# Kernel tuning notes

Hardware: AMD Instinct MI355X
Metric: run time of the kernel (lower is better)

Reference implementation:

```python
import jax, jax.numpy as jnp
import numpy as np
import math

B, T, E = 2, 2048, 1024
H = 16
D = E // H  # head_dim = 64

def setup_inputs() -> dict:
    key = jax.random.key(0)
    k1, k2, k3, k4, k5 = jax.random.split(key, 5)
    s = 0.02
    return {
        "x": jax.random.normal(k1, (B, T, E), dtype=jnp.float32),
        "W_attn": jax.random.normal(k2, (E, 3 * E), dtype=jnp.float32) * s,
        "b_attn": jax.random.normal(k3, (3 * E,), dtype=jnp.float32) * s,
        "W_proj": jax.random.normal(k4, (E, E), dtype=jnp.float32) * s,
        "b_proj": jax.random.normal(k5, (E,), dtype=jnp.float32) * s,
    }

def reference(x, W_attn, b_attn, W_proj, b_proj):
    Bx, Tx, Ex = x.shape
    qkv = x @ W_attn + b_attn                      # [B,T,3E]
    q, k, v = jnp.split(qkv, 3, axis=2)
    # [B,T,E] -> [B,H,T,D]
    def heads(t):
        return t.reshape(Bx, Tx, H, D).transpose(0, 2, 1, 3)
    q, k, v = heads(q), heads(k), heads(v)
    scores = jnp.einsum('bhqd,bhkd->bhqk', q, k) / math.sqrt(D)
    causal = jnp.tril(jnp.ones((Tx, Tx), dtype=bool))
    scores = jnp.where(causal, scores, -jnp.inf)
    attn = jax.nn.softmax(scores, axis=-1)
    out = jnp.einsum('bhqk,bhkd->bhqd', attn, v)   # [B,H,T,D]
    out = out.transpose(0, 2, 1, 3).reshape(Bx, Tx, Ex)
    return out @ W_proj + b_proj
```

## Files before the change

### kernel.cpp

```cpp
#include <hip/hip_runtime.h>


typedef unsigned short u16;
typedef __bf16 bf8 __attribute__((ext_vector_type(8)));
typedef float f32x4 __attribute__((ext_vector_type(4)));

struct __align__(8) u16x4s { u16 v[4]; };

__device__ __forceinline__ u16 f2b(float f) {
    union { float f; unsigned u; } x{f};
    unsigned r = x.u + 0x7fffu + ((x.u >> 16) & 1u);
    return (u16)(r >> 16);
}

__device__ __forceinline__ f32x4 mfma16(bf8 a, bf8 b, f32x4 c) {
    return __builtin_amdgcn_mfma_f32_16x16x32_bf16(a, b, c, 0, 0, 0);
}

__device__ __forceinline__ float fexp2(float x) {
    return __builtin_amdgcn_exp2f(x);
}

__device__ __forceinline__ void gload_lds16(const u16* g, u16* l) {
    __builtin_amdgcn_global_load_lds(
        (__attribute__((address_space(1))) void*)(g),
        (__attribute__((address_space(3))) void*)(l), 16, 0, 0);
}

__global__ __launch_bounds__(256) void k_prep(const float* __restrict__ x,
                                              const float* __restrict__ Wa,
                                              const float* __restrict__ Wp,
                                              u16* __restrict__ Xb,
                                              u16* __restrict__ WtA,
                                              u16* __restrict__ WtP) {
    __shared__ float tile[64][65];
    int id = blockIdx.x, t = threadIdx.x;
    if (id < 4096) {
        int i = id * 256 + t;
        float4 v = ((const float4*)x)[i];
        ushort4 o;
        o.x = f2b(v.x); o.y = f2b(v.y); o.z = f2b(v.z); o.w = f2b(v.w);
        ((ushort4*)Xb)[i] = o;
        return;
    }
    const float* in; u16* out; int N, j;
    if (id < 4864) { j = id - 4096; in = Wa; out = WtA; N = 3072; }
    else           { j = id - 4864; in = Wp; out = WtP; N = 1024; }
    int k0 = (j & 15) * 64, n0 = (j >> 4) * 64;
    int c = t & 63, r0 = t >> 6;
#pragma unroll
    for (int i = 0; i < 16; ++i) {
        int r = r0 + i * 4;
        tile[r][c] = in[(size_t)(k0 + r) * N + n0 + c];
    }
    __syncthreads();
#pragma unroll
    for (int i = 0; i < 16; ++i) {
        int r = r0 + i * 4;
        out[(size_t)(n0 + r) * 1024 + k0 + c] = f2b(tile[c][r]);
    }
}

#define GEMM_STAGE(GA0, GA1, GB0, GB1, K, B)                                   \
    do {                                                                       \
        gload_lds16(GA0 + (K), As[B] + tid * 8);                               \
        gload_lds16(GA1 + (K), As[B] + (256 + tid) * 8);                       \
        gload_lds16(GB0 + (K), Bs[B] + tid * 8);                               \
        gload_lds16(GB1 + (K), Bs[B] + (256 + tid) * 8);                       \
    } while (0)

#define GEMM_CORE(Aptr, Bptr)                                                  \
    int tid = threadIdx.x;                                                     \
    int w = tid >> 6, lane = tid & 63, l16 = lane & 15, quad = lane >> 4;      \
    int m0 = blockIdx.x * 128, n0 = blockIdx.y * 128;                          \
    int wr = (w >> 1) * 64, wc = (w & 1) * 64;                                 \
    __shared__ u16 As[2][128 * 32];                                            \
    __shared__ u16 Bs[2][128 * 32];                                            \
    f32x4 acc[4][4];                                                           \
    _Pragma("unroll") for (int mi = 0; mi < 4; ++mi)                           \
        _Pragma("unroll") for (int ni = 0; ni < 4; ++ni)                       \
            _Pragma("unroll") for (int r = 0; r < 4; ++r) acc[mi][ni][r] = 0.f;\
    int srow0 = tid >> 2, srow1 = 64 + srow0;                                  \
    int slc = ((tid & 3) ^ ((tid >> 3) & 3)) * 8;      \
    const u16* gA0 = Aptr + (size_t)(m0 + srow0) * 1024 + slc;                 \
    const u16* gA1 = Aptr + (size_t)(m0 + srow1) * 1024 + slc;                 \
    const u16* gB0 = Bptr + (size_t)(n0 + srow0) * 1024 + slc;                 \
    const u16* gB1 = Bptr + (size_t)(n0 + srow1) * 1024 + slc;                 \
    int cq = (quad ^ ((l16 >> 1) & 3)) * 8;               \
    GEMM_STAGE(gA0, gA1, gB0, gB1, 0, 0);                                      \
    for (int it = 0; it < 32; ++it) {                                          \
        int pb = it & 1;                                                       \
        __syncthreads();                           \
        bf8 af[4], bf[4];                                                      \
        _Pragma("unroll") for (int mi = 0; mi < 4; ++mi)                       \
            af[mi] = *(const bf8*)(As[pb] + (wr + mi * 16 + l16) * 32 + cq);   \
        _Pragma("unroll") for (int ni = 0; ni < 4; ++ni)                       \
            bf[ni] = *(const bf8*)(Bs[pb] + (wc + ni * 16 + l16) * 32 + cq);   \
        if (it < 31) GEMM_STAGE(gA0, gA1, gB0, gB1, (it + 1) * 32, pb ^ 1);    \
        _Pragma("unroll") for (int mi = 0; mi < 4; ++mi)                       \
            _Pragma("unroll") for (int ni = 0; ni < 4; ++ni)                   \
                acc[mi][ni] = mfma16(af[mi], bf[ni], acc[mi][ni]);             \
    }

__global__ __launch_bounds__(256, 3) void k_qkv(const u16* __restrict__ Xb,
                                                const u16* __restrict__ WtA,
                                                const float* __restrict__ ba,
                                                u16* __restrict__ Qb,
                                                u16* __restrict__ Kb,
                                                u16* __restrict__ Vtb) {
    GEMM_CORE(Xb, WtA)
    int sel = n0 >> 10;
    u16* dst = sel == 0 ? Qb : (sel == 1 ? Kb : Vtb);
    const float qs = 0.18033688011112042f;
#pragma unroll
    for (int ni = 0; ni < 4; ++ni) {
        int n = n0 + wc + ni * 16 + l16;
        float bias = ba[n];
        int h = (n & 1023) >> 6;
        int d = n & 63;
#pragma unroll
        for (int mi = 0; mi < 4; ++mi)
#pragma unroll
            for (int r = 0; r < 4; ++r) {
                int m = m0 + wr + mi * 16 + quad * 4 + r;
                int bb = m >> 11, tt = m & 2047;
                float v = acc[mi][ni][r] + bias;
                size_t hb = (size_t)(bb * 16 + h);
                if (sel == 2)
                    dst[hb * 131072 + (size_t)(tt >> 6) * 4096 + d * 64 + (tt & 63)] = f2b(v);
                else
                    dst[(hb * 2048 + tt) * 64 + d] =
                        f2b(sel == 0 ? v * qs : v);
            }
    }
}

__global__ __launch_bounds__(256, 3) void k_proj(const u16* __restrict__ AO,
                                                 const u16* __restrict__ WtP,
                                                 const float* __restrict__ bp,
                                                 float* __restrict__ out) {
    GEMM_CORE(AO, WtP)
#pragma unroll
    for (int ni = 0; ni < 4; ++ni) {
        int n = n0 + wc + ni * 16 + l16;
        float bias = bp[n];
#pragma unroll
        for (int mi = 0; mi < 4; ++mi)
#pragma unroll
            for (int r = 0; r < 4; ++r) {
                int m = m0 + wr + mi * 16 + quad * 4 + r;
                out[(size_t)m * 1024 + n] = acc[mi][ni][r] + bias;
            }
    }
}


#define STAGE(KT, B) do {                                                     \
    int ci0_ = tid, ci1_ = 256 + tid;                                         \
    const u16* kt_ = Kh + (size_t)(KT) * 4096;                                \
    gload_lds16(kt_ + (ci0_ >> 3) * 64 +                                      \
                (((ci0_ & 7) ^ ((ci0_ >> 5) & 7)) * 8), Ks[B] + ci0_ * 8);    \
    gload_lds16(kt_ + (ci1_ >> 3) * 64 +                                      \
                (((ci1_ & 7) ^ ((ci1_ >> 5) & 7)) * 8), Ks[B] + ci1_ * 8);    \
    const u16* vt_ = Vh + (size_t)(KT) * 4096;                                \
    gload_lds16(vt_ + (ci0_ >> 3) * 64 +                                      \
                (((ci0_ & 7) ^ ((ci0_ >> 3) & 7)) * 8), Vs[B] + ci0_ * 8);    \
    gload_lds16(vt_ + (ci1_ >> 3) * 64 +                                      \
                (((ci1_ & 7) ^ ((ci1_ >> 3) & 7)) * 8), Vs[B] + ci1_ * 8);    \
} while (0)

#define QK_SOFT(KT, KF, QF0, QF1, LI, QROW, KTM, PBUF) do {                   \
    int kb_ = (KT) * 64;                                                      \
    bool diag_ = ((KT) == (KTM));                                             \
    f32x4 s_acc[4];                                                           \
    _Pragma("unroll") for (int s = 0; s < 4; ++s)                             \
        _Pragma("unroll") for (int r = 0; r < 4; ++r) s_acc[s][r] = 0.f;      \
    _Pragma("unroll") for (int sub = 0; sub < 4; ++sub) {                     \
        s_acc[sub] = mfma16(QF0, KF[sub][0], s_acc[sub]);                     \
        s_acc[sub] = mfma16(QF1, KF[sub][1], s_acc[sub]);                     \
    }                                                                         \
    _Pragma("unroll") for (int r = 0; r < 4; ++r) {                           \
        float p[4];                                                           \
        if (diag_) {                                                          \
            int qg_ = (QROW) + quad * 4 + r;                                  \
            _Pragma("unroll") for (int sub = 0; sub < 4; ++sub) {             \
                int key_ = kb_ + 4 * l16 + sub;                               \
                p[sub] = fexp2(key_ <= qg_ ? s_acc[sub][r] : -1e30f);         \
            }                                                                 \
        } else {                                                              \
            _Pragma("unroll") for (int sub = 0; sub < 4; ++sub)               \
                p[sub] = fexp2(s_acc[sub][r]);                                \
        }                                                                     \
        LI[r] += (p[0] + p[1]) + (p[2] + p[3]);                               \
        u16x4s pk_;                                                           \
        _Pragma("unroll") for (int sub = 0; sub < 4; ++sub)                   \
            pk_.v[sub] = f2b(p[sub]);                                         \
        *(u16x4s*)&PBUF[quad * 4 + r][l16 * 4] = pk_;       \
    }                                                                         \
} while (0)

#define PV_ACC(VF, PBUF, OACC) do {                                           \
    bf8 pf0 = *(const bf8*)&PBUF[l16][quad * 8];                              \
    bf8 pf1 = *(const bf8*)&PBUF[l16][32 + quad * 8];                         \
    _Pragma("unroll") for (int dt = 0; dt < 4; ++dt) {                        \
        OACC[dt] = mfma16(pf0, VF[dt][0], OACC[dt]);                          \
        OACC[dt] = mfma16(pf1, VF[dt][1], OACC[dt]);                          \
    }                                                                         \
} while (0)

__global__ __launch_bounds__(256, 2) void k_attn(const u16* __restrict__ Qb,
                                                 const u16* __restrict__ Kb,
                                                 const u16* __restrict__ Vtb,
                                                 u16* __restrict__ AO) {
    int id = blockIdx.x;
    int bh = (id & 7) * 4 + ((id >> 3) & 3);
    int t  = 15 - (id >> 5);
    int tid = threadIdx.x;
    int w = tid >> 6, lane = tid & 63, l16 = lane & 15, quad = lane >> 4;

    const u16* Qh = Qb  + (size_t)bh * 2048 * 64;
    const u16* Kh = Kb  + (size_t)bh * 2048 * 64;
    const u16* Vh = Vtb + (size_t)bh * 131072;

    int qrA = t * 64 + w * 16;
    int qrB = qrA + 1024;
    int ktmaxA = t, ktmaxB = t + 16;

    __shared__ u16 Ks[2][64 * 64];
    __shared__ u16 Vs[2][64 * 64];
    __shared__ u16 P[4][2][16][72];

    bf8 qfA0 = *(const bf8*)(Qh + (size_t)(qrA + l16) * 64 + quad * 8);
    bf8 qfA1 = *(const bf8*)(Qh + (size_t)(qrA + l16) * 64 + 32 + quad * 8);
    bf8 qfB0 = *(const bf8*)(Qh + (size_t)(qrB + l16) * 64 + quad * 8);
    bf8 qfB1 = *(const bf8*)(Qh + (size_t)(qrB + l16) * 64 + 32 + quad * 8);

    float l_iA[4] = {0.f, 0.f, 0.f, 0.f};
    float l_iB[4] = {0.f, 0.f, 0.f, 0.f};
    f32x4 o_accA[4], o_accB[4];
#pragma unroll
    for (int dt = 0; dt < 4; ++dt)
#pragma unroll
        for (int r = 0; r < 4; ++r) { o_accA[dt][r] = 0.f; o_accB[dt][r] = 0.f; }

    int xsw = (l16 & 7) * 8;

    STAGE(0, 0);
    for (int kt = 0; kt <= ktmaxB; ++kt) {
        int pb = kt & 1;
        __syncthreads();

        bf8 kf[4][2], vf[4][2];
        const u16* kb_ = Ks[pb];
        const u16* vb_ = Vs[pb];
#pragma unroll
        for (int sub = 0; sub < 4; ++sub)
#pragma unroll
            for (int ks = 0; ks < 2; ++ks)
                kf[sub][ks] = *(const bf8*)(kb_ + (4 * l16 + sub) * 64 +
                                            (((ks * 32 + quad * 8)) ^ xsw));
#pragma unroll
        for (int dt = 0; dt < 4; ++dt)
#pragma unroll
            for (int ks = 0; ks < 2; ++ks)
                vf[dt][ks] = *(const bf8*)(vb_ + (dt * 16 + l16) * 64 +
                                           (((ks * 32 + quad * 8)) ^ xsw));

        if (kt < ktmaxB) STAGE(kt + 1, pb ^ 1);

        bool aAct = (kt <= ktmaxA);
        if (aAct) QK_SOFT(kt, kf, qfA0, qfA1, l_iA, qrA, ktmaxA, P[w][0]);
        QK_SOFT(kt, kf, qfB0, qfB1, l_iB, qrB, ktmaxB, P[w][1]);
        asm volatile("s_waitcnt lgkmcnt(0)" ::: "memory");
        if (aAct) PV_ACC(vf, P[w][0], o_accA);
        PV_ACC(vf, P[w][1], o_accB);
    }

    float linvA[4], linvB[4];
#pragma unroll
    for (int r = 0; r < 4; ++r) {
        float la = l_iA[r], lb = l_iB[r];
        la += __shfl_xor(la, 1, 64); lb += __shfl_xor(lb, 1, 64);
        la += __shfl_xor(la, 2, 64); lb += __shfl_xor(lb, 2, 64);
        la += __shfl_xor(la, 4, 64); lb += __shfl_xor(lb, 4, 64);
        la += __shfl_xor(la, 8, 64); lb += __shfl_xor(lb, 8, 64);
        linvA[r] = __builtin_amdgcn_rcpf(la);
        linvB[r] = __builtin_amdgcn_rcpf(lb);
    }

    int b = bh >> 4, h = bh & 15;
#pragma unroll
    for (int dt = 0; dt < 4; ++dt)
#pragma unroll
        for (int r = 0; r < 4; ++r) {
            int off = quad * 4 + r;
            size_t rowA = (size_t)b * 2048 + qrA + off;
            size_t rowB = (size_t)b * 2048 + qrB + off;
            AO[rowA * 1024 + h * 64 + dt * 16 + l16] = f2b(o_accA[dt][r] * linvA[r]);
            AO[rowB * 1024 + h * 64 + dt * 16 + l16] = f2b(o_accB[dt][r] * linvB[r]);
        }
}

extern "C" void kernel_launch(void* const* d_in, const int* in_sizes, int n_in,
                              void* d_out, int out_size, void* d_ws, size_t ws_size,
                              hipStream_t stream) {
    const float* x  = (const float*)d_in[0];
    const float* Wa = (const float*)d_in[1];
    const float* ba = (const float*)d_in[2];
    const float* Wp = (const float*)d_in[3];
    const float* bp = (const float*)d_in[4];
    float* out = (float*)d_out;

    char* ws = (char*)d_ws;
    const size_t MB = 1024 * 1024;
    u16* Xb  = (u16*)(ws);
    u16* WtA = (u16*)(ws + 8  * MB);
    u16* WtP = (u16*)(ws + 14 * MB);
    u16* Qb  = (u16*)(ws + 16 * MB);
    u16* Kb  = (u16*)(ws + 24 * MB);
    u16* Vtb = (u16*)(ws + 32 * MB);
    u16* AO  = Xb;

    k_prep<<<dim3(5120),    dim3(256), 0, stream>>>(x, Wa, Wp, Xb, WtA, WtP);
    k_qkv <<<dim3(32, 24),  dim3(256), 0, stream>>>(Xb, WtA, ba, Qb, Kb, Vtb);
    k_attn<<<dim3(512),     dim3(256), 0, stream>>>(Qb, Kb, Vtb, AO);
    k_proj<<<dim3(32, 8),   dim3(256), 0, stream>>>(AO, WtP, bp, out);
}
```

Before: 176.5 us.

## Load K/V fragments directly from global into registers, dropping LDS staging

The attention kernel no longer stages K and V tiles through double-buffered shared memory with barriers. Each wave now loads its K and V MFMA fragments straight from global memory into registers, prefetching the next K tile with a register double-buffer in an unrolled-by-two loop, and the __syncthreads is removed. The P scratch buffer is shrunk and XOR-swizzled to avoid bank conflicts, and the bf16 conversion uses the builtin cast. Every wave now reads K/V from global or L2 independently instead of sharing one LDS copy per block, which raises global traffic and register pressure in exchange for removing barriers and LDS round-trips.

```diff
diff --git a/kernel.cpp b/kernel.cpp
--- a/kernel.cpp
+++ b/kernel.cpp
@@ -8,9 +8,7 @@
 struct __align__(8) u16x4s { u16 v[4]; };
 
 __device__ __forceinline__ u16 f2b(float f) {
-    union { float f; unsigned u; } x{f};
-    unsigned r = x.u + 0x7fffu + ((x.u >> 16) & 1u);
-    return (u16)(r >> 16);
+    return __builtin_bit_cast(u16, (__bf16)f);
 }
 
 __device__ __forceinline__ f32x4 mfma16(bf8 a, bf8 b, f32x4 c) {
@@ -155,18 +153,18 @@
 }
 
 
-#define STAGE(KT, B) do {                                                     \
-    int ci0_ = tid, ci1_ = 256 + tid;                                         \
-    const u16* kt_ = Kh + (size_t)(KT) * 4096;                                \
-    gload_lds16(kt_ + (ci0_ >> 3) * 64 +                                      \
-                (((ci0_ & 7) ^ ((ci0_ >> 5) & 7)) * 8), Ks[B] + ci0_ * 8);    \
-    gload_lds16(kt_ + (ci1_ >> 3) * 64 +                                      \
-                (((ci1_ & 7) ^ ((ci1_ >> 5) & 7)) * 8), Ks[B] + ci1_ * 8);    \
-    const u16* vt_ = Vh + (size_t)(KT) * 4096;                                \
-    gload_lds16(vt_ + (ci0_ >> 3) * 64 +                                      \
-                (((ci0_ & 7) ^ ((ci0_ >> 3) & 7)) * 8), Vs[B] + ci0_ * 8);    \
-    gload_lds16(vt_ + (ci1_ >> 3) * 64 +                                      \
-                (((ci1_ & 7) ^ ((ci1_ >> 3) & 7)) * 8), Vs[B] + ci1_ * 8);    \
+#define LOADK(DST, KT) do {                                                   \
+    const u16* kp_ = Kh + (size_t)(KT) * 4096 + (4 * l16) * 64 + quad * 8;    \
+    _Pragma("unroll") for (int sub = 0; sub < 4; ++sub)                       \
+        _Pragma("unroll") for (int ks = 0; ks < 2; ++ks)                      \
+            DST[sub][ks] = *(const bf8*)(kp_ + sub * 64 + ks * 32);           \
+} while (0)
+
+#define LOADV(DST, KT) do {                                                   \
+    const u16* vp_ = Vh + (size_t)(KT) * 4096 + l16 * 64 + quad * 8;          \
+    _Pragma("unroll") for (int dt = 0; dt < 4; ++dt)                          \
+        _Pragma("unroll") for (int ks = 0; ks < 2; ++ks)                      \
+            DST[dt][ks] = *(const bf8*)(vp_ + dt * 1024 + ks * 32);           \
 } while (0)
 
 #define QK_SOFT(KT, KF, QF0, QF1, LI, QROW, KTM, PBUF) do {                   \
@@ -195,17 +193,31 @@
         u16x4s pk_;                                                           \
         _Pragma("unroll") for (int sub = 0; sub < 4; ++sub)                   \
             pk_.v[sub] = f2b(p[sub]);                                         \
-        *(u16x4s*)&PBUF[quad * 4 + r][l16 * 4] = pk_;       \
+        int prow_ = quad * 4 + r;                                             \
+        *(u16x4s*)&PBUF[prow_][(((l16 >> 1) ^ (prow_ & 7)) << 3) +            \
+                               ((l16 & 1) << 2)] = pk_;     \
     }                                                                         \
 } while (0)
 
 #define PV_ACC(VF, PBUF, OACC) do {                                           \
-    bf8 pf0 = *(const bf8*)&PBUF[l16][quad * 8];                              \
-    bf8 pf1 = *(const bf8*)&PBUF[l16][32 + quad * 8];                         \
+    int xp_ = l16 & 7;                                                        \
+    bf8 pf0 = *(const bf8*)&PBUF[l16][(quad ^ xp_) << 3];                     \
+    bf8 pf1 = *(const bf8*)&PBUF[l16][((4 + quad) ^ xp_) << 3];               \
     _Pragma("unroll") for (int dt = 0; dt < 4; ++dt) {                        \
         OACC[dt] = mfma16(pf0, VF[dt][0], OACC[dt]);                          \
         OACC[dt] = mfma16(pf1, VF[dt][1], OACC[dt]);                          \
     }                                                                         \
+} while (0)
+
+#define ATTN_BODY(KT, KC, KN) do {                                            \
+    if ((KT) + 1 <= ktmaxB) LOADK(KN, (KT) + 1);                              \
+    LOADV(vf, KT);                                                            \
+    bool aAct_ = ((KT) <= ktmaxA);                                            \
+    if (aAct_) QK_SOFT(KT, KC, qfA0, qfA1, l_iA, qrA, ktmaxA, P[w][0]);       \
+    QK_SOFT(KT, KC, qfB0, qfB1, l_iB, qrB, ktmaxB, P[w][1]);                  \
+    asm volatile("s_waitcnt lgkmcnt(0)" ::: "memory");     \
+    if (aAct_) PV_ACC(vf, P[w][0], o_accA);                                   \
+    PV_ACC(vf, P[w][1], o_accB);                                              \
 } while (0)
 
 __global__ __launch_bounds__(256, 2) void k_attn(const u16* __restrict__ Qb,
@@ -226,9 +238,7 @@
     int qrB = qrA + 1024;
     int ktmaxA = t, ktmaxB = t + 16;
 
-    __shared__ u16 Ks[2][64 * 64];
-    __shared__ u16 Vs[2][64 * 64];
-    __shared__ u16 P[4][2][16][72];
+    __shared__ u16 P[4][2][16][64];
 
     bf8 qfA0 = *(const bf8*)(Qh + (size_t)(qrA + l16) * 64 + quad * 8);
     bf8 qfA1 = *(const bf8*)(Qh + (size_t)(qrA + l16) * 64 + 32 + quad * 8);
@@ -243,38 +253,15 @@
 #pragma unroll
         for (int r = 0; r < 4; ++r) { o_accA[dt][r] = 0.f; o_accB[dt][r] = 0.f; }
 
-    int xsw = (l16 & 7) * 8;
-
-    STAGE(0, 0);
-    for (int kt = 0; kt <= ktmaxB; ++kt) {
-        int pb = kt & 1;
-        __syncthreads();
-
-        bf8 kf[4][2], vf[4][2];
-        const u16* kb_ = Ks[pb];
-        const u16* vb_ = Vs[pb];
-#pragma unroll
-        for (int sub = 0; sub < 4; ++sub)
-#pragma unroll
-            for (int ks = 0; ks < 2; ++ks)
-                kf[sub][ks] = *(const bf8*)(kb_ + (4 * l16 + sub) * 64 +
-                                            (((ks * 32 + quad * 8)) ^ xsw));
-#pragma unroll
-        for (int dt = 0; dt < 4; ++dt)
-#pragma unroll
-            for (int ks = 0; ks < 2; ++ks)
-                vf[dt][ks] = *(const bf8*)(vb_ + (dt * 16 + l16) * 64 +
-                                           (((ks * 32 + quad * 8)) ^ xsw));
-
-        if (kt < ktmaxB) STAGE(kt + 1, pb ^ 1);
-
-        bool aAct = (kt <= ktmaxA);
-        if (aAct) QK_SOFT(kt, kf, qfA0, qfA1, l_iA, qrA, ktmaxA, P[w][0]);
-        QK_SOFT(kt, kf, qfB0, qfB1, l_iB, qrB, ktmaxB, P[w][1]);
-        asm volatile("s_waitcnt lgkmcnt(0)" ::: "memory");
-        if (aAct) PV_ACC(vf, P[w][0], o_accA);
-        PV_ACC(vf, P[w][1], o_accB);
-    }
+    bf8 kf0[4][2], kf1[4][2], vf[4][2];
+    LOADK(kf0, 0);
+    int nkt = ktmaxB + 1;
+    int kt = 0;
+    for (; kt + 1 < nkt; kt += 2) {
+        ATTN_BODY(kt,     kf0, kf1);
+        ATTN_BODY(kt + 1, kf1, kf0);
+    }
+    if (kt < nkt) ATTN_BODY(kt, kf0, kf1);
 
     float linvA[4], linvB[4];
 #pragma unroll
```

New measurement: 241.3 us. 1.37x slower.
